# Kernel tuning notes

Hardware: AMD Instinct MI355X
Metric: run time of the kernel (lower is better)

## Reference

```python
import jax, jax.numpy as jnp
import numpy as np

N = 100000   # total nodes (batched molecules)
E = 250000   # directed edges
B = 2000     # number of graphs
F_IN = 75    # atom feature dim
DIM = 32     # hidden dim


def setup_inputs() -> dict:
    key = jax.random.key(0)
    ks = jax.random.split(key, 12)
    def gl(k, shape, fan_in):
        return (jax.random.normal(k, shape, jnp.float32) / np.sqrt(fan_in)).astype(jnp.float32)
    inp = {}
    inp['node_features'] = jax.random.normal(ks[0], (N, F_IN), jnp.float32)
    inp['edge_features'] = jax.random.normal(ks[1], (E, 11), jnp.float32)
    inp['lin0_w'] = gl(ks[2], (DIM, F_IN), F_IN)
    inp['lin0_b'] = jnp.zeros((DIM,), jnp.float32)
    # edge network: Linear(11,128) -> ReLU -> Linear(128, DIM*DIM)
    inp['nn_w1'] = gl(ks[3], (128, 11), 11)
    inp['nn_b1'] = jnp.zeros((128,), jnp.float32)
    inp['nn_w2'] = gl(ks[4], (DIM * DIM, 128), 128)
    inp['nn_b2'] = jnp.zeros((DIM * DIM,), jnp.float32)
    inp['conv_bias'] = jnp.zeros((DIM,), jnp.float32)  # NNConv bias (root_weight=False)
    # GRU(dim, dim), torch gate order: r, z, n
    inp['gru_wih'] = gl(ks[5], (3 * DIM, DIM), DIM)
    inp['gru_whh'] = gl(ks[6], (3 * DIM, DIM), DIM)
    inp['gru_bih'] = jnp.zeros((3 * DIM,), jnp.float32)
    inp['gru_bhh'] = jnp.zeros((3 * DIM,), jnp.float32)
    # Set2Set LSTM(2*dim, dim), torch gate order: i, f, g, o
    inp['lstm_wih'] = gl(ks[7], (4 * DIM, 2 * DIM), 2 * DIM)
    inp['lstm_whh'] = gl(ks[8], (4 * DIM, DIM), DIM)
    inp['lstm_bih'] = jnp.zeros((4 * DIM,), jnp.float32)
    inp['lstm_bhh'] = jnp.zeros((4 * DIM,), jnp.float32)
    inp['edge_index'] = jax.random.randint(ks[9], (2, E), 0, N)
    inp['graph_index'] = jnp.sort(jax.random.randint(ks[10], (N,), 0, B))
    return inp


def _nnconv(x, edge_w, src, dst, bias):
    # per-edge: gather src features, apply [dim,dim] edge weight, scatter-mean to dst
    msg = jnp.einsum('ei,eio->eo', x[src], edge_w)           # [E, DIM]
    s = jax.ops.segment_sum(msg, dst, num_segments=N)         # [N, DIM]
    cnt = jax.ops.segment_sum(jnp.ones((msg.shape[0],), msg.dtype), dst, num_segments=N)
    mean = s / jnp.maximum(cnt, 1.0)[:, None]
    return mean + bias


def _gru_cell(x, h, wih, whh, bih, bhh):
    gi = x @ wih.T + bih
    gh = h @ whh.T + bhh
    gi_r, gi_z, gi_n = jnp.split(gi, 3, axis=-1)
    gh_r, gh_z, gh_n = jnp.split(gh, 3, axis=-1)
    r = jax.nn.sigmoid(gi_r + gh_r)
    z = jax.nn.sigmoid(gi_z + gh_z)
    n = jnp.tanh(gi_n + r * gh_n)
    return (1.0 - z) * n + z * h


def _lstm_cell(x, h, c, wih, whh, bih, bhh):
    g = x @ wih.T + bih + h @ whh.T + bhh
    i, f, gg, o = jnp.split(g, 4, axis=-1)
    c = jax.nn.sigmoid(f) * c + jax.nn.sigmoid(i) * jnp.tanh(gg)
    h = jax.nn.sigmoid(o) * jnp.tanh(c)
    return h, c


def _set2set(x, batch, wih, whh, bih, bhh, steps=3):
    dim = x.shape[-1]
    h = jnp.zeros((B, dim), x.dtype)
    c = jnp.zeros((B, dim), x.dtype)
    q_star = jnp.zeros((B, 2 * dim), x.dtype)
    for _ in range(steps):
        q, c = _lstm_cell(q_star, h, c, wih, whh, bih, bhh)
        h = q
        e = jnp.sum(x * q[batch], axis=-1)                    # [N]
        emax = jax.ops.segment_max(e, batch, num_segments=B)
        ex = jnp.exp(e - emax[batch])
        denom = jax.ops.segment_sum(ex, batch, num_segments=B)
        a = ex / denom[batch]
        r = jax.ops.segment_sum(a[:, None] * x, batch, num_segments=B)
        q_star = jnp.concatenate([q, r], axis=-1)
    return q_star


def reference(node_features, edge_features, lin0_w, lin0_b, nn_w1, nn_b1, nn_w2, nn_b2,
              conv_bias, gru_wih, gru_whh, gru_bih, gru_bhh,
              lstm_wih, lstm_whh, lstm_bih, lstm_bhh, edge_index, graph_index):
    src, dst = edge_index[0], edge_index[1]
    out = jax.nn.relu(node_features @ lin0_w.T + lin0_b)      # [N, DIM]
    # edge network (edge_features are fixed -> identical every iteration)
    hw = jax.nn.relu(edge_features @ nn_w1.T + nn_b1)
    edge_w = (hw @ nn_w2.T + nn_b2).reshape(-1, DIM, DIM)     # [E, DIM, DIM]
    h = out
    for _ in range(3):
        m = jax.nn.relu(_nnconv(out, edge_w, src, dst, conv_bias))
        h = _gru_cell(m, h, gru_wih, gru_whh, gru_bih, gru_bhh)
        out = h
    pooled = _set2set(out, graph_index, lstm_wih, lstm_whh, lstm_bih, lstm_bhh)
    return pooled, out
```

## Files before the change

### kernel.cpp

```cpp
#include <hip/hip_runtime.h>
#include <stdint.h>

#define N_NODES  100000
#define N_EDGES  250000
#define N_GRAPHS 2000
#define F_IN     75
#define DIM      32
#define H1       128

#define MSG_BLOCKS 977
#define CH        8
#define NSTAGES   17
#define KT_PAD    (CH * NSTAGES)
#define W2F_HALFS (KT_PAD * 1024)

#define CNT_BLOCKS  ((N_EDGES + 255) / 256)
#define OFFS_BLOCKS ((N_NODES + 255) / 256)
#define GRUW_BLOCKS 32

typedef _Float16 v8h __attribute__((ext_vector_type(8)));
typedef float    v4f __attribute__((ext_vector_type(4)));

__device__ __forceinline__ void gld_lds16(const void* g, void* l) {
    __builtin_amdgcn_global_load_lds(
        (const __attribute__((address_space(1))) unsigned int*)g,
        (__attribute__((address_space(3))) unsigned int*)l, 16, 0, 0);
}

__global__ __launch_bounds__(256) void lin0_kernel(
    const float* __restrict__ nf, const float* __restrict__ w,
    const float* __restrict__ b, _Float16* __restrict__ h16) {
    __shared__ float wl[DIM * F_IN];
    __shared__ float bl[DIM];
    int t = threadIdx.x;
    for (int i = t; i < DIM * F_IN; i += 256) wl[i] = w[i];
    if (t < DIM) bl[t] = b[t];
    __syncthreads();
    int nl = t >> 5, o = t & 31;
    #pragma unroll
    for (int p = 0; p < 4; ++p) {
        int n = blockIdx.x * 32 + p * 8 + nl;
        if (n >= N_NODES) continue;
        const float* row = nf + (size_t)n * F_IN;
        float acc = bl[o];
        #pragma unroll
        for (int i = 0; i < F_IN; ++i) acc += row[i] * wl[o * F_IN + i];
        h16[(size_t)n * DIM + o] = (_Float16)fmaxf(acc, 0.f);
    }
}

__global__ __launch_bounds__(256) void prep_w2f_kernel(
    const float* __restrict__ w2, const float* __restrict__ b2,
    _Float16* __restrict__ w2f) {
    int id = blockIdx.x * 256 + threadIdx.x;
    if (id >= W2F_HALFS) return;
    int j    = id & 7;
    int lane = (id >> 3) & 63;
    int ng   = (id >> 9) & 1;
    int kt   = id >> 10;
    int lr = lane & 15, q = lane >> 4;
    int c = kt * 32 + q * 8 + j;
    int o = ng * 16 + lr;
    float val = 0.f;
    if (c < 4096)      val = w2[((c >> 7) * 32 + o) * H1 + (c & 127)];
    else if (c < 4128) val = b2[(c - 4096) * 32 + o];
    w2f[id] = (_Float16)val;
}

__global__ __launch_bounds__(256) void hw_kernel(
    const float* __restrict__ ef, const float* __restrict__ w1,
    const float* __restrict__ b1, _Float16* __restrict__ hwf,
    int e_off) {
    __shared__ float wl[H1 * 11];
    __shared__ float bl[H1];
    int t = threadIdx.x;
    for (int i = t; i < H1 * 11; i += 256) wl[i] = w1[i];
    if (t < H1) bl[t] = b1[t];
    __syncthreads();
    int k = t & 127;
    #pragma unroll
    for (int p = 0; p < 16; ++p) {
        int le = blockIdx.x * 32 + p * 2 + (t >> 7);
        int e  = e_off + le;
        float acc = 0.f;
        if (e < N_EDGES) {
            const float* row = ef + (size_t)e * 11;
            acc = bl[k];
            #pragma unroll
            for (int i = 0; i < 11; ++i) acc += row[i] * wl[k * 11 + i];
            acc = fmaxf(acc, 0.f);
        }
        size_t addr = (size_t)(le >> 4) * 2048 + (k >> 3) * 128 + (le & 15) * 8 + (k & 7);
        hwf[addr] = (_Float16)acc;
    }
}

__global__ __launch_bounds__(256) void aux_kernel(
    const int* __restrict__ dst, float* __restrict__ cnt,
    const int* __restrict__ gidx, int* __restrict__ gstart,
    const float* __restrict__ wih, const float* __restrict__ whh,
    _Float16* __restrict__ gw) {
    int t = threadIdx.x;
    if (blockIdx.x < CNT_BLOCKS) {
        int e = blockIdx.x * 256 + t;
        if (e < N_EDGES) atomicAdd(&cnt[dst[e]], 1.0f);
    } else if (blockIdx.x < CNT_BLOCKS + OFFS_BLOCKS) {
        int n = (blockIdx.x - CNT_BLOCKS) * 256 + t;
        if (n >= N_NODES) return;
        int b = gidx[n];
        if (n == 0) {
            for (int bb = 0; bb <= b; ++bb) gstart[bb] = 0;
        } else {
            int a = gidx[n - 1];
            for (int bb = a + 1; bb <= b; ++bb) gstart[bb] = n;
        }
        if (n == N_NODES - 1) {
            for (int bb = b + 1; bb <= N_GRAPHS; ++bb) gstart[bb] = N_NODES;
        }
    } else {
        int id = (blockIdx.x - CNT_BLOCKS - OFFS_BLOCKS) * 256 + t;
        if (id >= 8192) return;
        int im = id & 4095;
        int r = im / 40, c = im - r * 40;
        float val = 0.f;
        if (r < 96 && c < 32) val = (id < 4096) ? wih[r * 32 + c] : whh[r * 32 + c];
        gw[id] = (_Float16)val;
    }
}

__global__ __launch_bounds__(256) void msg_kernel(
    const _Float16* __restrict__ hwf, const _Float16* __restrict__ w2f,
    const _Float16* __restrict__ x16, const int* __restrict__ src,
    const int* __restrict__ dst, float* __restrict__ sbuf, int e_off) {
    __shared__ _Float16 xs[32 * 256];
    __shared__ _Float16 bst[2][CH * 1024];

    int t = threadIdx.x;
    int w = t >> 6, lane = t & 63, lr = lane & 15, q = lane >> 4;
    int wbase = w * 64;

    {
        const char* gp = (const char*)w2f;
        char* lp = (char*)&bst[0][0];
        #pragma unroll
        for (int it = 0; it < 4; ++it)
            gld_lds16(gp + it * 4096 + t * 16, lp + it * 4096 + t * 16);
    }

    v8h hwr[4][4];
    {
        const v8h* hv = (const v8h*)hwf;
        int T0 = blockIdx.x * 16 + w * 4;
        #pragma unroll
        for (int mt = 0; mt < 4; ++mt)
            #pragma unroll
            for (int kc = 0; kc < 4; ++kc)
                hwr[mt][kc] = hv[(size_t)(T0 + mt) * 256 + (kc * 4 + q) * 16 + lr];
    }

    {
        int e = e_off + blockIdx.x * 256 + t;
        int ec = e < N_EDGES ? e : N_EDGES - 1;
        int sv = src[ec];
        const v8h* xr = (const v8h*)(x16 + (size_t)sv * DIM);
        #pragma unroll
        for (int u = 0; u < 4; ++u) {
            v8h v = xr[u];
            #pragma unroll
            for (int j = 0; j < 8; ++j)
                xs[(u * 8 + j) * 256 + t] = v[j];
        }
    }
    __syncthreads();

    v4f acc[4][2];
    #pragma unroll
    for (int mt = 0; mt < 4; ++mt)
        #pragma unroll
        for (int ng = 0; ng < 2; ++ng) { v4f z = {0.f, 0.f, 0.f, 0.f}; acc[mt][ng] = z; }

    _Float16 xsc[4];

    for (int s = 0; s < NSTAGES - 1; ++s) {
        {
            const char* gp = (const char*)(w2f + (size_t)(s + 1) * CH * 1024);
            char* lp = (char*)&bst[(s + 1) & 1][0];
            #pragma unroll
            for (int it = 0; it < 4; ++it)
                gld_lds16(gp + it * 4096 + t * 16, lp + it * 4096 + t * 16);
        }
        const _Float16* bb = &bst[s & 1][0];
        #pragma unroll
        for (int ktl = 0; ktl < CH; ++ktl) {
            int kt = s * CH + ktl;
            v8h b0 = *(const v8h*)(bb + ktl * 1024 + lane * 8);
            v8h b1 = *(const v8h*)(bb + ktl * 1024 + 512 + lane * 8);
            if ((kt & 3) == 0) {
                int i = kt >> 2;
                #pragma unroll
                for (int mt = 0; mt < 4; ++mt)
                    xsc[mt] = xs[i * 256 + wbase + mt * 16 + lr];
            }
            int kc = kt & 3;
            #pragma unroll
            for (int mt = 0; mt < 4; ++mt) {
                v8h a = hwr[mt][kc] * xsc[mt];
                acc[mt][0] = __builtin_amdgcn_mfma_f32_16x16x32_f16(a, b0, acc[mt][0], 0, 0, 0);
                acc[mt][1] = __builtin_amdgcn_mfma_f32_16x16x32_f16(a, b1, acc[mt][1], 0, 0, 0);
            }
        }
        __syncthreads();
    }
    {
        const _Float16* bb = &bst[0][0];
        v8h b0 = *(const v8h*)(bb + lane * 8);
        v8h b1 = *(const v8h*)(bb + 512 + lane * 8);
        #pragma unroll
        for (int mt = 0; mt < 4; ++mt) {
            v8h a;
            #pragma unroll
            for (int j = 0; j < 8; ++j)
                a[j] = xs[(q * 8 + j) * 256 + wbase + mt * 16 + lr];
            acc[mt][0] = __builtin_amdgcn_mfma_f32_16x16x32_f16(a, b0, acc[mt][0], 0, 0, 0);
            acc[mt][1] = __builtin_amdgcn_mfma_f32_16x16x32_f16(a, b1, acc[mt][1], 0, 0, 0);
        }
    }

    int E0 = e_off + blockIdx.x * 256 + wbase;
    #pragma unroll
    for (int mt = 0; mt < 4; ++mt) {
        #pragma unroll
        for (int r = 0; r < 4; ++r) {
            int e = E0 + mt * 16 + q * 4 + r;
            if (e < N_EDGES) {
                int dv = dst[e];
                float* sp = sbuf + (size_t)dv * DIM;
                atomicAdd(sp + lr,      acc[mt][0][r]);
                atomicAdd(sp + 16 + lr, acc[mt][1][r]);
            }
        }
    }
}

__global__ __launch_bounds__(256) void gru_kernel(
    float* __restrict__ s, const float* __restrict__ cnt,
    const float* __restrict__ cb, const _Float16* __restrict__ gw,
    const float* __restrict__ bih, const float* __restrict__ bhh,
    _Float16* __restrict__ h16, float* __restrict__ hout, int last) {
    __shared__ _Float16 wi_l[4096], wh_l[4096];
    __shared__ float bi_l[96], bh_l[96];
    __shared__ _Float16 m_l[128 * 32], h_l[128 * 32];
    int t = threadIdx.x;

    {
        const char* gp = (const char*)gw;
        gld_lds16(gp + t * 16,         (char*)wi_l + t * 16);
        gld_lds16(gp + 4096 + t * 16,  (char*)wi_l + 4096 + t * 16);
        gld_lds16(gp + 8192 + t * 16,  (char*)wh_l + t * 16);
        gld_lds16(gp + 12288 + t * 16, (char*)wh_l + 4096 + t * 16);
    }
    if (t < 96) { bi_l[t] = bih[t]; bh_l[t] = bhh[t]; }

    {
        int node_l = t >> 1, part = t & 1;
        int n = blockIdx.x * 128 + node_l;
        int nc = n < N_NODES ? n : N_NODES - 1;
        float c = cnt[nc];
        float rc = 1.f / (c > 1.f ? c : 1.f);
        float4* s4 = (float4*)(s + (size_t)nc * DIM + part * 16);
        const float* cbp = cb + part * 16;
        #pragma unroll
        for (int u = 0; u < 2; ++u) {
            float4 sa = s4[u * 2], sb = s4[u * 2 + 1];
            v8h mv;
            mv[0] = (_Float16)fmaxf(sa.x * rc + cbp[u * 8 + 0], 0.f);
            mv[1] = (_Float16)fmaxf(sa.y * rc + cbp[u * 8 + 1], 0.f);
            mv[2] = (_Float16)fmaxf(sa.z * rc + cbp[u * 8 + 2], 0.f);
            mv[3] = (_Float16)fmaxf(sa.w * rc + cbp[u * 8 + 3], 0.f);
            mv[4] = (_Float16)fmaxf(sb.x * rc + cbp[u * 8 + 4], 0.f);
            mv[5] = (_Float16)fmaxf(sb.y * rc + cbp[u * 8 + 5], 0.f);
            mv[6] = (_Float16)fmaxf(sb.z * rc + cbp[u * 8 + 6], 0.f);
            mv[7] = (_Float16)fmaxf(sb.w * rc + cbp[u * 8 + 7], 0.f);
            *(v8h*)&m_l[node_l * 32 + part * 16 + u * 8] = mv;
        }
        if (n < N_NODES) {
            float4 z4 = {0.f, 0.f, 0.f, 0.f};
            s4[0] = z4; s4[1] = z4; s4[2] = z4; s4[3] = z4;
        }
        const v8h* h8 = (const v8h*)(h16 + (size_t)nc * DIM + part * 16);
        *(v8h*)&h_l[node_l * 32 + part * 16]     = h8[0];
        *(v8h*)&h_l[node_l * 32 + part * 16 + 8] = h8[1];
    }

    __syncthreads();

    int w = t >> 6, lane = t & 63, lr = lane & 15, q = lane >> 4;

    v8h bi6[6], bh6[6];
    #pragma unroll
    for (int nt = 0; nt < 6; ++nt) {
        bi6[nt] = *(const v8h*)&wi_l[(nt * 16 + lr) * 40 + q * 8];
        bh6[nt] = *(const v8h*)&wh_l[(nt * 16 + lr) * 40 + q * 8];
    }

    #pragma unroll
    for (int p = 0; p < 2; ++p) {
        int tb = w * 32 + p * 16;
        v4f ai[6], ah[6];
        #pragma unroll
        for (int nt = 0; nt < 6; ++nt) {
            float bii = bi_l[nt * 16 + lr], bhi = bh_l[nt * 16 + lr];
            v4f ci = {bii, bii, bii, bii}; ai[nt] = ci;
            v4f chh = {bhi, bhi, bhi, bhi}; ah[nt] = chh;
        }
        v8h ma = *(const v8h*)&m_l[(tb + lr) * 32 + q * 8];
        v8h ha = *(const v8h*)&h_l[(tb + lr) * 32 + q * 8];
        #pragma unroll
        for (int nt = 0; nt < 6; ++nt) {
            ai[nt] = __builtin_amdgcn_mfma_f32_16x16x32_f16(ma, bi6[nt], ai[nt], 0, 0, 0);
            ah[nt] = __builtin_amdgcn_mfma_f32_16x16x32_f16(ha, bh6[nt], ah[nt], 0, 0, 0);
        }
        int nb = blockIdx.x * 128 + tb + q * 4;
        #pragma unroll
        for (int g = 0; g < 2; ++g) {
            int o = g * 16 + lr;
            #pragma unroll
            for (int r = 0; r < 4; ++r) {
                int n2 = nb + r;
                if (n2 < N_NODES) {
                    float rg = 1.f / (1.f + expf(-(ai[g][r]     + ah[g][r])));
                    float zg = 1.f / (1.f + expf(-(ai[2 + g][r] + ah[2 + g][r])));
                    float ng = tanhf(ai[4 + g][r] + rg * ah[4 + g][r]);
                    float hold = (float)h_l[(tb + q * 4 + r) * 32 + o];
                    float hn = (1.f - zg) * ng + zg * hold;
                    h16[(size_t)n2 * DIM + o] = (_Float16)hn;
                    if (last) hout[(size_t)n2 * DIM + o] = hn;
                }
            }
        }
    }
}

__global__ __launch_bounds__(256) void s2s_kernel(
    const float* __restrict__ wih, const float* __restrict__ whh,
    const float* __restrict__ bih, const float* __restrict__ bhh,
    float* __restrict__ h, float* __restrict__ c,
    float* __restrict__ rnum, float* __restrict__ denom,
    const float* __restrict__ x, const int* __restrict__ gstart,
    float* __restrict__ outp, int first, int wout) {
    __shared__ float wA[128 * 33], wB[128 * 33], bl[128];
    int t = threadIdx.x;
    for (int i = t; i < 128 * 32; i += 256) {
        int r = i >> 5, cc = i & 31;
        wA[r * 33 + cc] = wih[r * 64 + cc] + whh[r * 32 + cc];
        wB[r * 33 + cc] = wih[r * 64 + 32 + cc];
    }
    if (t < 128) bl[t] = bih[t] + bhh[t];
    __syncthreads();
    int gl = t >> 5, o = t & 31;
    int b = blockIdx.x * 8 + gl;
    if (b >= N_GRAPHS) return;

    float hq = 0.f, rr = 0.f, cv = 0.f;
    if (!first) {
        hq = h[b * DIM + o];
        float d = denom[b];
        rr = d > 0.f ? rnum[b * DIM + o] / d : 0.f;
        cv = c[b * DIM + o];
    }
    float gi = bl[o], gf = bl[32 + o], gg = bl[64 + o], go = bl[96 + o];
    #pragma unroll
    for (int i = 0; i < 32; ++i) {
        float qv = __shfl(hq, i, 32);
        float rv = __shfl(rr, i, 32);
        gi += qv * wA[o * 33 + i]        + rv * wB[o * 33 + i];
        gf += qv * wA[(32 + o) * 33 + i] + rv * wB[(32 + o) * 33 + i];
        gg += qv * wA[(64 + o) * 33 + i] + rv * wB[(64 + o) * 33 + i];
        go += qv * wA[(96 + o) * 33 + i] + rv * wB[(96 + o) * 33 + i];
    }
    float si = 1.f / (1.f + expf(-gi));
    float sf = 1.f / (1.f + expf(-gf));
    float so = 1.f / (1.f + expf(-go));
    float cn = sf * cv + si * tanhf(gg);
    float qo = so * tanhf(cn);
    c[b * DIM + o] = cn;
    h[b * DIM + o] = qo;

    int n0 = gstart[b], n1 = gstart[b + 1];
    float m0 = -3.0e38f, s = 0.f, r = 0.f;
    for (int n = n0; n < n1; ++n) {
        float xo = x[(size_t)n * DIM + o];
        float e = xo * qo;
        #pragma unroll
        for (int mm = 16; mm >= 1; mm >>= 1) e += __shfl_xor(e, mm, 32);
        float nm = fmaxf(m0, e);
        float sc = expf(m0 - nm);
        float ex = expf(e - nm);
        s = s * sc + ex;
        r = r * sc + ex * xo;
        m0 = nm;
    }
    rnum[b * DIM + o] = r;
    if (o == 0) denom[b] = s;
    if (wout) {
        outp[b * 64 + o]      = qo;
        outp[b * 64 + 32 + o] = s > 0.f ? r / s : 0.f;
    }
}

extern "C" void kernel_launch(void* const* d_in, const int* in_sizes, int n_in,
                              void* d_out, int out_size, void* d_ws, size_t ws_size,
                              hipStream_t stream) {
    const float* nf   = (const float*)d_in[0];
    const float* ef   = (const float*)d_in[1];
    const float* l0w  = (const float*)d_in[2];
    const float* l0b  = (const float*)d_in[3];
    const float* w1   = (const float*)d_in[4];
    const float* b1   = (const float*)d_in[5];
    const float* w2   = (const float*)d_in[6];
    const float* b2   = (const float*)d_in[7];
    const float* cb   = (const float*)d_in[8];
    const float* gwih = (const float*)d_in[9];
    const float* gwhh = (const float*)d_in[10];
    const float* gbih = (const float*)d_in[11];
    const float* gbhh = (const float*)d_in[12];
    const float* lwih = (const float*)d_in[13];
    const float* lwhh = (const float*)d_in[14];
    const float* lbih = (const float*)d_in[15];
    const float* lbhh = (const float*)d_in[16];
    const int*   eidx = (const int*)d_in[17];
    const int*   gidx = (const int*)d_in[18];
    const int* src = eidx;
    const int* dst = eidx + N_EDGES;
    float* out = (float*)d_out;
    float* h   = out + (size_t)N_GRAPHS * 64;

    char* ws = (char*)d_ws;
    size_t off = 0;
    auto alloc = [&](size_t bytes) -> void* {
        void* p = ws + off;
        off = (off + bytes + 255) & ~(size_t)255;
        return p;
    };
    float* sbuf  = (float*)alloc((size_t)N_NODES * DIM * 4);
    float* cnt   = (float*)alloc((size_t)N_NODES * 4);
    _Float16* h16 = (_Float16*)alloc((size_t)N_NODES * DIM * 2);
    float* hs    = (float*)alloc((size_t)N_GRAPHS * DIM * 4);
    float* cs    = (float*)alloc((size_t)N_GRAPHS * DIM * 4);
    float* rnum  = (float*)alloc((size_t)N_GRAPHS * DIM * 4);
    float* denom = (float*)alloc((size_t)N_GRAPHS * 4);
    int*   gstart = (int*)alloc((size_t)(N_GRAPHS + 1) * 4);
    _Float16* w2f  = (_Float16*)alloc((size_t)W2F_HALFS * 2);
    _Float16* gw   = (_Float16*)alloc((size_t)16384);
    size_t fixed = off;
    size_t avail = ws_size > fixed ? ws_size - fixed : 0;

    auto need = [&](int nc) -> size_t {
        int cbk = (MSG_BLOCKS + nc - 1) / nc;
        return (size_t)cbk * 16 * 4096;
    };
    int nchunk = 1;
    while (nchunk < 64 && need(nchunk) > avail) nchunk <<= 1;
    int chunk_blocks = (MSG_BLOCKS + nchunk - 1) / nchunk;
    _Float16* hwf = (_Float16*)alloc(need(nchunk));

    lin0_kernel<<<dim3((N_NODES + 31) / 32), dim3(256), 0, stream>>>(nf, l0w, l0b, h16);
    prep_w2f_kernel<<<dim3((W2F_HALFS + 255) / 256), dim3(256), 0, stream>>>(w2, b2, w2f);
    hipMemsetAsync(cnt, 0, (size_t)N_NODES * 4, stream);
    aux_kernel<<<dim3(CNT_BLOCKS + OFFS_BLOCKS + GRUW_BLOCKS), dim3(256), 0, stream>>>(
        dst, cnt, gidx, gstart, gwih, gwhh, gw);
    if (nchunk == 1) {
        hw_kernel<<<dim3(MSG_BLOCKS * 8), dim3(256), 0, stream>>>(ef, w1, b1, hwf, 0);
    }
    hipMemsetAsync(sbuf, 0, (size_t)N_NODES * DIM * 4, stream);

    for (int it = 0; it < 3; ++it) {
        for (int cix = 0; cix < nchunk; ++cix) {
            int bstart = cix * chunk_blocks;
            int bc = MSG_BLOCKS - bstart;
            if (bc <= 0) break;
            if (bc > chunk_blocks) bc = chunk_blocks;
            int e_off = bstart * 256;
            if (nchunk > 1)
                hw_kernel<<<dim3(bc * 8), dim3(256), 0, stream>>>(ef, w1, b1, hwf, e_off);
            msg_kernel<<<dim3(bc), dim3(256), 0, stream>>>(hwf, w2f, h16, src, dst, sbuf, e_off);
        }
        gru_kernel<<<dim3((N_NODES + 127) / 128), dim3(256), 0, stream>>>(
            sbuf, cnt, cb, gw, gbih, gbhh, h16, h, it == 2 ? 1 : 0);
    }

    for (int st = 0; st < 3; ++st) {
        s2s_kernel<<<dim3((N_GRAPHS + 7) / 8), dim3(256), 0, stream>>>(
            lwih, lwhh, lbih, lbhh, hs, cs, rnum, denom, h, gstart, out,
            st == 0 ? 1 : 0, st == 2 ? 1 : 0);
    }
}
```

Measured before the change: 595.9 us.

## Fuse setup kernels and memsets, vectorize hw_kernel, split s2s softmax across halves

Folds the cnt and sbuf zeroing into lin0_kernel and merges prep_w2f into aux_kernel, which removes two memsets and one launch. hw_kernel now stages edge features in LDS and writes 8-half vectors with 64 edges per block, cutting uncoalesced stores. s2s_kernel gives each graph two 32-lane halves that each walk alternate nodes, then merges their online-softmax state, which halves the serial per-graph loop. The cost is more complex fused kernels and fewer graphs per s2s block.

```diff
diff --git a/kernel.cpp b/kernel.cpp
--- a/kernel.cpp
+++ b/kernel.cpp
@@ -17,6 +17,7 @@
 #define CNT_BLOCKS  ((N_EDGES + 255) / 256)
 #define OFFS_BLOCKS ((N_NODES + 255) / 256)
 #define GRUW_BLOCKS 32
+#define W2F_BLOCKS  ((W2F_HALFS + 255) / 256)
 
 typedef _Float16 v8h __attribute__((ext_vector_type(8)));
 typedef float    v4f __attribute__((ext_vector_type(4)));
@@ -29,7 +30,8 @@
 
 __global__ __launch_bounds__(256) void lin0_kernel(
     const float* __restrict__ nf, const float* __restrict__ w,
-    const float* __restrict__ b, _Float16* __restrict__ h16) {
+    const float* __restrict__ b, _Float16* __restrict__ h16,
+    float* __restrict__ cnt, float* __restrict__ sbuf) {
     __shared__ float wl[DIM * F_IN];
     __shared__ float bl[DIM];
     int t = threadIdx.x;
@@ -47,51 +49,14 @@
         for (int i = 0; i < F_IN; ++i) acc += row[i] * wl[o * F_IN + i];
         h16[(size_t)n * DIM + o] = (_Float16)fmaxf(acc, 0.f);
     }
-}
-
-__global__ __launch_bounds__(256) void prep_w2f_kernel(
-    const float* __restrict__ w2, const float* __restrict__ b2,
-    _Float16* __restrict__ w2f) {
-    int id = blockIdx.x * 256 + threadIdx.x;
-    if (id >= W2F_HALFS) return;
-    int j    = id & 7;
-    int lane = (id >> 3) & 63;
-    int ng   = (id >> 9) & 1;
-    int kt   = id >> 10;
-    int lr = lane & 15, q = lane >> 4;
-    int c = kt * 32 + q * 8 + j;
-    int o = ng * 16 + lr;
-    float val = 0.f;
-    if (c < 4096)      val = w2[((c >> 7) * 32 + o) * H1 + (c & 127)];
-    else if (c < 4128) val = b2[(c - 4096) * 32 + o];
-    w2f[id] = (_Float16)val;
-}
-
-__global__ __launch_bounds__(256) void hw_kernel(
-    const float* __restrict__ ef, const float* __restrict__ w1,
-    const float* __restrict__ b1, _Float16* __restrict__ hwf,
-    int e_off) {
-    __shared__ float wl[H1 * 11];
-    __shared__ float bl[H1];
-    int t = threadIdx.x;
-    for (int i = t; i < H1 * 11; i += 256) wl[i] = w1[i];
-    if (t < H1) bl[t] = b1[t];
-    __syncthreads();
-    int k = t & 127;
-    #pragma unroll
-    for (int p = 0; p < 16; ++p) {
-        int le = blockIdx.x * 32 + p * 2 + (t >> 7);
-        int e  = e_off + le;
-        float acc = 0.f;
-        if (e < N_EDGES) {
-            const float* row = ef + (size_t)e * 11;
-            acc = bl[k];
-            #pragma unroll
-            for (int i = 0; i < 11; ++i) acc += row[i] * wl[k * 11 + i];
-            acc = fmaxf(acc, 0.f);
-        }
-        size_t addr = (size_t)(le >> 4) * 2048 + (k >> 3) * 128 + (le & 15) * 8 + (k & 7);
-        hwf[addr] = (_Float16)acc;
+    if (t < 32) {
+        int n = blockIdx.x * 32 + t;
+        if (n < N_NODES) cnt[n] = 0.f;
+    }
+    #pragma unroll
+    for (int p = 0; p < 4; ++p) {
+        size_t idx = (size_t)blockIdx.x * 1024 + p * 256 + t;
+        if (idx < (size_t)N_NODES * DIM) sbuf[idx] = 0.f;
     }
 }
 
@@ -99,13 +64,16 @@
     const int* __restrict__ dst, float* __restrict__ cnt,
     const int* __restrict__ gidx, int* __restrict__ gstart,
     const float* __restrict__ wih, const float* __restrict__ whh,
-    _Float16* __restrict__ gw) {
+    _Float16* __restrict__ gw,
+    const float* __restrict__ w2, const float* __restrict__ b2,
+    _Float16* __restrict__ w2f) {
     int t = threadIdx.x;
-    if (blockIdx.x < CNT_BLOCKS) {
-        int e = blockIdx.x * 256 + t;
+    unsigned bx = blockIdx.x;
+    if (bx < CNT_BLOCKS) {
+        int e = bx * 256 + t;
         if (e < N_EDGES) atomicAdd(&cnt[dst[e]], 1.0f);
-    } else if (blockIdx.x < CNT_BLOCKS + OFFS_BLOCKS) {
-        int n = (blockIdx.x - CNT_BLOCKS) * 256 + t;
+    } else if (bx < CNT_BLOCKS + OFFS_BLOCKS) {
+        int n = (bx - CNT_BLOCKS) * 256 + t;
         if (n >= N_NODES) return;
         int b = gidx[n];
         if (n == 0) {
@@ -117,14 +85,61 @@
         if (n == N_NODES - 1) {
             for (int bb = b + 1; bb <= N_GRAPHS; ++bb) gstart[bb] = N_NODES;
         }
-    } else {
-        int id = (blockIdx.x - CNT_BLOCKS - OFFS_BLOCKS) * 256 + t;
+    } else if (bx < CNT_BLOCKS + OFFS_BLOCKS + GRUW_BLOCKS) {
+        int id = (bx - CNT_BLOCKS - OFFS_BLOCKS) * 256 + t;
         if (id >= 8192) return;
         int im = id & 4095;
         int r = im / 40, c = im - r * 40;
         float val = 0.f;
         if (r < 96 && c < 32) val = (id < 4096) ? wih[r * 32 + c] : whh[r * 32 + c];
         gw[id] = (_Float16)val;
+    } else {
+        int id = (bx - CNT_BLOCKS - OFFS_BLOCKS - GRUW_BLOCKS) * 256 + t;
+        if (id >= W2F_HALFS) return;
+        int j    = id & 7;
+        int lane = (id >> 3) & 63;
+        int ng   = (id >> 9) & 1;
+        int kt   = id >> 10;
+        int lr = lane & 15, q = lane >> 4;
+        int c = kt * 32 + q * 8 + j;
+        int o = ng * 16 + lr;
+        float val = 0.f;
+        if (c < 4096)      val = w2[((c >> 7) * 32 + o) * H1 + (c & 127)];
+        else if (c < 4128) val = b2[(c - 4096) * 32 + o];
+        w2f[id] = (_Float16)val;
+    }
+}
+
+__global__ __launch_bounds__(256) void hw_kernel(
+    const float* __restrict__ ef, const float* __restrict__ w1,
+    const float* __restrict__ b1, _Float16* __restrict__ hwf,
+    int e_off) {
+    __shared__ float wl[H1 * 11];
+    __shared__ float bl[H1];
+    __shared__ float efl[64 * 11];
+    int t = threadIdx.x;
+    for (int i = t; i < H1 * 11; i += 256) wl[i] = w1[i];
+    if (t < H1) bl[t] = b1[t];
+    for (int i = t; i < 64 * 11; i += 256) {
+        int le = i / 11, j = i - le * 11;
+        int e = e_off + blockIdx.x * 64 + le;
+        efl[i] = e < N_EDGES ? ef[(size_t)e * 11 + j] : 0.f;
+    }
+    __syncthreads();
+    int le_l = t >> 4, kc8 = t & 15;
+    #pragma unroll
+    for (int p = 0; p < 4; ++p) {
+        const float* row = &efl[(p * 16 + le_l) * 11];
+        v8h outv;
+        #pragma unroll
+        for (int j = 0; j < 8; ++j) {
+            int k = kc8 * 8 + j;
+            float acc = bl[k];
+            #pragma unroll
+            for (int i = 0; i < 11; ++i) acc += row[i] * wl[k * 11 + i];
+            outv[j] = (_Float16)fmaxf(acc, 0.f);
+        }
+        *(v8h*)(hwf + (size_t)(blockIdx.x * 4 + p) * 2048 + kc8 * 128 + le_l * 8) = outv;
     }
 }
 
@@ -357,8 +372,8 @@
     }
     if (t < 128) bl[t] = bih[t] + bhh[t];
     __syncthreads();
-    int gl = t >> 5, o = t & 31;
-    int b = blockIdx.x * 8 + gl;
+    int gl = t >> 6, half = (t >> 5) & 1, o = t & 31;
+    int b = blockIdx.x * 4 + gl;
     if (b >= N_GRAPHS) return;
 
     float hq = 0.f, rr = 0.f, cv = 0.f;
@@ -383,12 +398,14 @@
     float so = 1.f / (1.f + expf(-go));
     float cn = sf * cv + si * tanhf(gg);
     float qo = so * tanhf(cn);
-    c[b * DIM + o] = cn;
-    h[b * DIM + o] = qo;
+    if (half == 0) {
+        c[b * DIM + o] = cn;
+        h[b * DIM + o] = qo;
+    }
 
     int n0 = gstart[b], n1 = gstart[b + 1];
     float m0 = -3.0e38f, s = 0.f, r = 0.f;
-    for (int n = n0; n < n1; ++n) {
+    for (int n = n0 + half; n < n1; n += 2) {
         float xo = x[(size_t)n * DIM + o];
         float e = xo * qo;
         #pragma unroll
@@ -400,11 +417,21 @@
         r = r * sc + ex * xo;
         m0 = nm;
     }
-    rnum[b * DIM + o] = r;
-    if (o == 0) denom[b] = s;
-    if (wout) {
-        outp[b * 64 + o]      = qo;
-        outp[b * 64 + 32 + o] = s > 0.f ? r / s : 0.f;
+    float vm = __shfl_xor(m0, 32);
+    float vs = __shfl_xor(s, 32);
+    float vr = __shfl_xor(r, 32);
+    float nm = fmaxf(m0, vm);
+    float sc0 = expf(m0 - nm), sc1 = expf(vm - nm);
+    s = s * sc0 + vs * sc1;
+    r = r * sc0 + vr * sc1;
+
+    if (half == 0) {
+        rnum[b * DIM + o] = r;
+        if (o == 0) denom[b] = s;
+        if (wout) {
+            outp[b * 64 + o]      = qo;
+            outp[b * 64 + 32 + o] = s > 0.f ? r / s : 0.f;
+        }
     }
 }
 
@@ -464,15 +491,13 @@
     int chunk_blocks = (MSG_BLOCKS + nchunk - 1) / nchunk;
     _Float16* hwf = (_Float16*)alloc(need(nchunk));
 
-    lin0_kernel<<<dim3((N_NODES + 31) / 32), dim3(256), 0, stream>>>(nf, l0w, l0b, h16);
-    prep_w2f_kernel<<<dim3((W2F_HALFS + 255) / 256), dim3(256), 0, stream>>>(w2, b2, w2f);
-    hipMemsetAsync(cnt, 0, (size_t)N_NODES * 4, stream);
-    aux_kernel<<<dim3(CNT_BLOCKS + OFFS_BLOCKS + GRUW_BLOCKS), dim3(256), 0, stream>>>(
-        dst, cnt, gidx, gstart, gwih, gwhh, gw);
+    lin0_kernel<<<dim3((N_NODES + 31) / 32), dim3(256), 0, stream>>>(
+        nf, l0w, l0b, h16, cnt, sbuf);
+    aux_kernel<<<dim3(CNT_BLOCKS + OFFS_BLOCKS + GRUW_BLOCKS + W2F_BLOCKS), dim3(256), 0, stream>>>(
+        dst, cnt, gidx, gstart, gwih, gwhh, gw, w2, b2, w2f);
     if (nchunk == 1) {
-        hw_kernel<<<dim3(MSG_BLOCKS * 8), dim3(256), 0, stream>>>(ef, w1, b1, hwf, 0);
-    }
-    hipMemsetAsync(sbuf, 0, (size_t)N_NODES * DIM * 4, stream);
+        hw_kernel<<<dim3((MSG_BLOCKS * 256 + 63) / 64), dim3(256), 0, stream>>>(ef, w1, b1, hwf, 0);
+    }
 
     for (int it = 0; it < 3; ++it) {
         for (int cix = 0; cix < nchunk; ++cix) {
@@ -482,7 +507,7 @@
             if (bc > chunk_blocks) bc = chunk_blocks;
             int e_off = bstart * 256;
             if (nchunk > 1)
-                hw_kernel<<<dim3(bc * 8), dim3(256), 0, stream>>>(ef, w1, b1, hwf, e_off);
+                hw_kernel<<<dim3(bc * 4), dim3(256), 0, stream>>>(ef, w1, b1, hwf, e_off);
             msg_kernel<<<dim3(bc), dim3(256), 0, stream>>>(hwf, w2f, h16, src, dst, sbuf, e_off);
         }
         gru_kernel<<<dim3((N_NODES + 127) / 128), dim3(256), 0, stream>>>(
@@ -490,7 +515,7 @@
     }
 
     for (int st = 0; st < 3; ++st) {
-        s2s_kernel<<<dim3((N_GRAPHS + 7) / 8), dim3(256), 0, stream>>>(
+        s2s_kernel<<<dim3((N_GRAPHS + 3) / 4), dim3(256), 0, stream>>>(
             lwih, lwhh, lbih, lbhh, hs, cs, rnum, denom, h, gstart, out,
             st == 0 ? 1 : 0, st == 2 ? 1 : 0);
     }
```

Result: no change. 607.5 us (+1.9%).
